# Kernel optimization log

Measured on AMD Instinct MI355X. Metric: run time of the kernel, lower is better.

The kernel has to match this reference:

```python
import jax, jax.numpy as jnp
import numpy as np

D = 1536          # d_model
H = 12            # n_heads // 2 for chunk attention
HD = D // H       # head dim = 128
MAXC = 256        # max_chunks
MAXLEN = 1024     # max_seq_length (size embedding table)
THRESH = 0.5      # boundary threshold (init value of the learned param)


def _gelu(v):
    return jax.nn.gelu(v, approximate=False)  # torch nn.GELU default (erf)


def _cos(a, b):
    # F.cosine_similarity with eps=1e-8
    na = jnp.maximum(jnp.linalg.norm(a, axis=-1), 1e-8)
    nb = jnp.maximum(jnp.linalg.norm(b, axis=-1), 1e-8)
    return jnp.sum(a * b, axis=-1) / (na * nb)


def _interp1d(y, L_out):
    # F.interpolate(mode='linear', align_corners=False) on [B, L_in] -> [B, L_out]
    L_in = y.shape[1]
    src = jnp.clip((jnp.arange(L_out, dtype=y.dtype) + 0.5) * (L_in / L_out) - 0.5, 0.0, L_in - 1)
    i0 = jnp.floor(src).astype(jnp.int32)
    i1 = jnp.minimum(i0 + 1, L_in - 1)
    w = src - i0.astype(y.dtype)
    return y[:, i0] * (1.0 - w) + y[:, i1] * w


def setup_inputs() -> dict:
    key = jax.random.key(0)
    ks = jax.random.split(key, 16)
    B, S = 4, 1024
    rn = lambda k, sh, s=0.02: jax.random.normal(k, sh, dtype=jnp.float32) * s
    return {
        'x': jax.random.normal(ks[0], (B, S, D), dtype=jnp.float32),
        'Wp': rn(ks[1], (D, D)), 'bp': jnp.zeros((D,), jnp.float32),
        'detW1': rn(ks[2], (3, D, 2 * D)), 'detb1': jnp.zeros((3, D), jnp.float32),
        'detW2': rn(ks[3], (3, D // 2, D)), 'detb2': jnp.zeros((3, D // 2), jnp.float32),
        'detW3': rn(ks[4], (3, D // 2)), 'detb3': jnp.zeros((3,), jnp.float32),
        'in_proj_w': rn(ks[5], (3 * D, D)), 'in_proj_b': jnp.zeros((3 * D,), jnp.float32),
        'out_w': rn(ks[6], (D, D)), 'out_b': jnp.zeros((D,), jnp.float32),
        'size_emb': jax.random.normal(ks[7], (MAXLEN, D), dtype=jnp.float32),
        'pos_enc': rn(ks[8], (1, MAXC, D)),
        'procW1': rn(ks[9], (2 * D, D)), 'procb1': jnp.zeros((2 * D,), jnp.float32),
        'procW2': rn(ks[10], (D, 2 * D)), 'procb2': jnp.zeros((D,), jnp.float32),
        'ln_g': jnp.ones((D,), jnp.float32), 'ln_b': jnp.zeros((D,), jnp.float32),
    }


def reference(x, Wp, bp, detW1, detb1, detW2, detb2, detW3, detb3,
              in_proj_w, in_proj_b, out_w, out_b, size_emb, pos_enc,
              procW1, procb1, procW2, procb2, ln_g, ln_b):
    B, S, d = x.shape
    # ---- DynamicSemanticChunker ----
    x_ling = x @ Wp.T + bp
    sims = []
    for scale in (1, 2, 4):
        xs = x_ling[:, ::scale]
        cs = _cos(xs[:, :-1], xs[:, 1:])           # [B, L-1]
        sims.append(_interp1d(cs, S - 1))           # [B, S-1]
    avg_sim = jnp.mean(jnp.stack(sims, 0), axis=0)
    base = 0.5 * (1.0 - avg_sim)
    bi = jnp.concatenate([x[:, :-1], x[:, 1:]], axis=-1)  # [B, S-1, 2d]
    h1 = _gelu(jnp.einsum('bsk,ndk->nbsd', bi, detW1) + detb1[:, None, None, :])
    h2 = _gelu(jnp.einsum('nbsd,nhd->nbsh', h1, detW2) + detb2[:, None, None, :])
    learned = jax.nn.sigmoid(jnp.einsum('nbsh,nh->nbs', h2, detW3) + detb3[:, None, None])
    avg_learned = jnp.mean(learned, axis=0)
    final = 0.6 * base + 0.4 * avg_learned
    boundaries = jnp.concatenate([jnp.ones((B, 1), x.dtype), final], axis=1)  # [B, S]
    # ---- EnhancedChunkLayer.create_chunks ----
    # contiguous ragged chunks == segments between boundary positions
    seg = jnp.cumsum((boundaries > THRESH).astype(jnp.int32), axis=1) - 1      # [B, S]
    # per-chunk MHA == full-seq attention with block-diagonal same-segment mask
    qkv = x @ in_proj_w.T + in_proj_b
    q, k, v = jnp.split(qkv, 3, axis=-1)
    q = q.reshape(B, S, H, HD)
    k = k.reshape(B, S, H, HD)
    v = v.reshape(B, S, H, HD)
    scores = jnp.einsum('bqhd,bkhd->bhqk', q, k) / np.sqrt(HD).astype(np.float32)
    same = (seg[:, None, :, None] == seg[:, None, None, :])                    # [B,1,S,S]
    scores = jnp.where(same, scores, jnp.asarray(-1e9, scores.dtype))
    attn = jax.nn.softmax(scores, axis=-1)
    ctx = jnp.einsum('bhqk,bkhd->bqhd', attn, v).reshape(B, S, d)
    attn_out = ctx @ out_w.T + out_b                                           # [B, S, d]
    # masked segment mean pooling; chunks with id >= MAXC are truncated away
    onehot = (seg[..., None] == jnp.arange(MAXC)).astype(x.dtype)              # [B,S,MAXC]
    sums = jnp.einsum('bsm,bsd->bmd', onehot, attn_out)
    counts = jnp.sum(onehot, axis=1)                                            # [B,MAXC]
    mean = sums / jnp.maximum(counts, 1.0)[..., None]
    clen = jnp.minimum(counts.astype(jnp.int32), MAXLEN - 1)
    sizes = size_emb[clen]                                                      # [B,MAXC,d]
    chunk = jnp.where(counts[..., None] > 0, mean + sizes, 0.0)                 # zero-pad empty
    # ---- pos encoding + chunk_processor (Linear->GELU->Linear->LayerNorm) ----
    chunk = chunk + pos_enc
    h = _gelu(chunk @ procW1.T + procb1)
    y = h @ procW2.T + procb2
    mu = jnp.mean(y, axis=-1, keepdims=True)
    var = jnp.var(y, axis=-1, keepdims=True)
    y = (y - mu) / jnp.sqrt(var + 1e-5) * ln_g + ln_b
    return y  # [B, MAXC, d]
```

## Files before the change

kernel.cpp:

```cpp
#include <hip/hip_runtime.h>
#include <hip/hip_bf16.h>
#include <math.h>

#define D_ 1536
#define S_ 1024
#define B_ 4
#define H_ 12
#define HD_ 128
#define MAXC_ 256

typedef __bf16 bf16x8_t __attribute__((ext_vector_type(8)));
typedef float f32x4_t __attribute__((ext_vector_type(4)));

__device__ __forceinline__ float gelu_f(float v) {
    return 0.5f * v * (1.0f + erff(v / 1.41421356237f));
}

__device__ __forceinline__ void split2(float a, __hip_bfloat16& h, __hip_bfloat16& l) {
    h = __float2bfloat16(a);
    l = __float2bfloat16(a - __bfloat162float(h));
}

__device__ __forceinline__ void xcd_swizzle(int& bx, int& by, int gx, int gy) {
    int nwg = gx * gy;
    int orig = by * gx + bx;
    int xcd = orig & 7;
    int q = nwg >> 3, r = nwg & 7;
    int wg = (xcd < r ? xcd * (q + 1) : r * (q + 1) + (xcd - r) * q) + (orig >> 3);
    bx = wg % gx;
    by = wg / gx;
}

template<int BM, int SPLITA, int SPLITB, int ACT, int OUT, int DBUF>
__global__ __launch_bounds__(256, 2)
void mfma3_gemm(const float* __restrict__ Af, const __hip_bfloat16* __restrict__ Ah,
                const __hip_bfloat16* __restrict__ Al,
                const float* __restrict__ Bf, const __hip_bfloat16* __restrict__ Bh,
                const __hip_bfloat16* __restrict__ Bl,
                const float* __restrict__ bias, int biasStride,
                float* __restrict__ Cf, __hip_bfloat16* __restrict__ Ch, __hip_bfloat16* __restrict__ Cl,
                const float* __restrict__ w3, float* __restrict__ lg,
                int K, int lda, int ldb, int ldc,
                long long aBound, long long azS, long long bzS, long long czS)
{
    constexpr int NB = DBUF ? 2 : 1;
    __shared__ __align__(16) __hip_bfloat16 Ash[NB][BM * 32], Asl[NB][BM * 32];
    __shared__ __align__(16) __hip_bfloat16 Bsh[NB][128 * 32], Bsl[NB][128 * 32];
    const int z = blockIdx.z;
    int bxi = blockIdx.x, byi = blockIdx.y;
    xcd_swizzle(bxi, byi, gridDim.x, gridDim.y);
    const int bm = byi * BM, bn = bxi * 128;
    const int tid = threadIdx.x, lane = tid & 63, wave = tid >> 6;
    const int wm = (BM == 128) ? (wave >> 1) : 0;
    const int wn = (BM == 128) ? (wave & 1) : wave;
    constexpr int NF = (BM == 128) ? 4 : 2;
    constexpr int WC = NF * 16;
    const int fr = lane & 15, kg = lane >> 4;
    f32x4_t acc[4][NF] = {};
    constexpr int RSH = (BM == 128) ? 1 : 2;
    constexpr int NBA = (BM == 128) ? 2 : 1;
    const int ar = tid >> RSH, akb = tid & ((1 << RSH) - 1);
    const int br = tid >> 1, bkb = tid & 1;

    bf16x8_t rAh[NBA], rAl[NBA], rBh[2], rBl[2];
    float4 rAf[NBA][2], rBf[2][2];

    auto load_tile = [&](int k0) {
        #pragma unroll
        for (int j = 0; j < NBA; ++j) {
            int skg = akb * NBA + j;
            long long base = (long long)(bm + ar) * lda + azS * z + k0 + skg * 8;
            if (SPLITA) {
                #pragma unroll
                for (int q = 0; q < 2; ++q) {
                    float4 v = make_float4(0.f, 0.f, 0.f, 0.f);
                    if (base + q * 4 + 4 <= aBound) v = *reinterpret_cast<const float4*>(&Af[base + q * 4]);
                    rAf[j][q] = v;
                }
            } else {
                rAh[j] = *reinterpret_cast<const bf16x8_t*>(&Ah[base]);
                rAl[j] = *reinterpret_cast<const bf16x8_t*>(&Al[base]);
            }
        }
        #pragma unroll
        for (int j = 0; j < 2; ++j) {
            int skg = bkb * 2 + j;
            long long base = (long long)(bn + br) * ldb + bzS * z + k0 + skg * 8;
            if (SPLITB) {
                #pragma unroll
                for (int q = 0; q < 2; ++q)
                    rBf[j][q] = *reinterpret_cast<const float4*>(&Bf[base + q * 4]);
            } else {
                rBh[j] = *reinterpret_cast<const bf16x8_t*>(&Bh[base]);
                rBl[j] = *reinterpret_cast<const bf16x8_t*>(&Bl[base]);
            }
        }
    };

    auto write_tile = [&](int buf) {
        #pragma unroll
        for (int j = 0; j < NBA; ++j) {
            int skg = akb * NBA + j;
            int blk = ar * 4 + (skg ^ ((ar >> 1) & 3));
            if (SPLITA) {
                float av[8];
                *reinterpret_cast<float4*>(&av[0]) = rAf[j][0];
                *reinterpret_cast<float4*>(&av[4]) = rAf[j][1];
                __hip_bfloat16 hh[8], ll[8];
                #pragma unroll
                for (int q = 0; q < 8; ++q) split2(av[q], hh[q], ll[q]);
                *reinterpret_cast<bf16x8_t*>(&Ash[buf][blk * 8]) = *reinterpret_cast<bf16x8_t*>(hh);
                *reinterpret_cast<bf16x8_t*>(&Asl[buf][blk * 8]) = *reinterpret_cast<bf16x8_t*>(ll);
            } else {
                *reinterpret_cast<bf16x8_t*>(&Ash[buf][blk * 8]) = rAh[j];
                *reinterpret_cast<bf16x8_t*>(&Asl[buf][blk * 8]) = rAl[j];
            }
        }
        #pragma unroll
        for (int j = 0; j < 2; ++j) {
            int skg = bkb * 2 + j;
            int blk = br * 4 + (skg ^ ((br >> 1) & 3));
            if (SPLITB) {
                float av[8];
                *reinterpret_cast<float4*>(&av[0]) = rBf[j][0];
                *reinterpret_cast<float4*>(&av[4]) = rBf[j][1];
                __hip_bfloat16 hh[8], ll[8];
                #pragma unroll
                for (int q = 0; q < 8; ++q) split2(av[q], hh[q], ll[q]);
                *reinterpret_cast<bf16x8_t*>(&Bsh[buf][blk * 8]) = *reinterpret_cast<bf16x8_t*>(hh);
                *reinterpret_cast<bf16x8_t*>(&Bsl[buf][blk * 8]) = *reinterpret_cast<bf16x8_t*>(ll);
            } else {
                *reinterpret_cast<bf16x8_t*>(&Bsh[buf][blk * 8]) = rBh[j];
                *reinterpret_cast<bf16x8_t*>(&Bsl[buf][blk * 8]) = rBl[j];
            }
        }
    };

    load_tile(0);
    write_tile(0);
    __syncthreads();
    int cur = 0;

    for (int k0 = 0; k0 < K; k0 += 32) {
        const bool has_next = (k0 + 32) < K;
        if (has_next) load_tile(k0 + 32);

        bf16x8_t fah[4], fal[4], fbh[NF], fbl[NF];
        #pragma unroll
        for (int m = 0; m < 4; ++m) {
            int row = wm * 64 + m * 16 + fr;
            int blk = row * 4 + (kg ^ ((row >> 1) & 3));
            fah[m] = *reinterpret_cast<const bf16x8_t*>(&Ash[cur][blk * 8]);
            fal[m] = *reinterpret_cast<const bf16x8_t*>(&Asl[cur][blk * 8]);
        }
        #pragma unroll
        for (int n = 0; n < NF; ++n) {
            int row = wn * WC + n * 16 + fr;
            int blk = row * 4 + (kg ^ ((row >> 1) & 3));
            fbh[n] = *reinterpret_cast<const bf16x8_t*>(&Bsh[cur][blk * 8]);
            fbl[n] = *reinterpret_cast<const bf16x8_t*>(&Bsl[cur][blk * 8]);
        }
        #pragma unroll
        for (int m = 0; m < 4; ++m)
            #pragma unroll
            for (int n = 0; n < NF; ++n) {
                acc[m][n] = __builtin_amdgcn_mfma_f32_16x16x32_bf16(fah[m], fbh[n], acc[m][n], 0, 0, 0);
                acc[m][n] = __builtin_amdgcn_mfma_f32_16x16x32_bf16(fah[m], fbl[n], acc[m][n], 0, 0, 0);
                acc[m][n] = __builtin_amdgcn_mfma_f32_16x16x32_bf16(fal[m], fbh[n], acc[m][n], 0, 0, 0);
            }

        if (has_next) {
            if (DBUF) {
                write_tile(cur ^ 1);
                __syncthreads();
                cur ^= 1;
            } else {
                __syncthreads();
                write_tile(0);
                __syncthreads();
            }
        }
    }

    const int fq = lane >> 4;
    const float* bp_ = bias + (long long)biasStride * z;

    if constexpr (OUT == 2) {
        float psum[4][4] = {};
        #pragma unroll
        for (int n = 0; n < NF; ++n) {
            int col = bn + wn * WC + n * 16 + fr;
            float bv = bp_[col];
            float wv = w3[(long long)biasStride * z + col];
            #pragma unroll
            for (int m = 0; m < 4; ++m)
                #pragma unroll
                for (int r = 0; r < 4; ++r) {
                    float v = acc[m][n][r] + bv;
                    v = gelu_f(v);
                    psum[m][r] += v * wv;
                }
        }
        #pragma unroll
        for (int m = 0; m < 4; ++m)
            #pragma unroll
            for (int r = 0; r < 4; ++r) {
                float p = psum[m][r];
                p += __shfl_xor(p, 1);
                p += __shfl_xor(p, 2);
                p += __shfl_xor(p, 4);
                p += __shfl_xor(p, 8);
                if (fr == 0) {
                    int row = bm + wm * 64 + m * 16 + fq * 4 + r;
                    atomicAdd(&lg[czS * z + row], p);
                }
            }
        return;
    }

    #pragma unroll
    for (int n = 0; n < NF; ++n) {
        int col = bn + wn * WC + n * 16 + fr;
        float bv = bp_[col];
        #pragma unroll
        for (int m = 0; m < 4; ++m) {
            int row0 = bm + wm * 64 + m * 16 + fq * 4;
            #pragma unroll
            for (int r = 0; r < 4; ++r) {
                float v = acc[m][n][r] + bv;
                if (ACT == 1) v = gelu_f(v);
                long long ci = czS * z + (long long)(row0 + r) * ldc + col;
                if constexpr (OUT == 0) {
                    Cf[ci] = v;
                } else {
                    __hip_bfloat16 hh, ll;
                    split2(v, hh, ll);
                    Ch[ci] = hh; Cl[ci] = ll;
                }
            }
        }
    }
}

template<int ACT, int OUT_BF16>
__global__ __launch_bounds__(256)
void mfma_gemm(const __hip_bfloat16* __restrict__ A, const __hip_bfloat16* __restrict__ Bw,
               const float* __restrict__ bias, void* __restrict__ Cout,
               int M, int N, int K)
{
    __shared__ __align__(16) __hip_bfloat16 As[2][128 * 32];
    __shared__ __align__(16) __hip_bfloat16 Bs[2][128 * 32];
    const int tid = threadIdx.x;
    const int lane = tid & 63;
    const int wave = tid >> 6;
    const int wm = wave >> 1, wn = wave & 1;
    int bxi = blockIdx.x, byi = blockIdx.y;
    xcd_swizzle(bxi, byi, gridDim.x, gridDim.y);
    const int bm = byi * 128, bn = bxi * 128;
    const int srow = tid >> 2;
    const int skg = tid & 3;
    const int fr = lane & 15, kg = lane >> 4;

    f32x4_t acc[4][4] = {};
    bf16x8_t rA[2], rB[2];

    auto load_tile = [&](int k0) {
        #pragma unroll
        for (int it = 0; it < 2; ++it) {
            int r = srow + it * 64;
            rA[it] = *reinterpret_cast<const bf16x8_t*>(&A[(long long)(bm + r) * K + k0 + skg * 8]);
            rB[it] = *reinterpret_cast<const bf16x8_t*>(&Bw[(long long)(bn + r) * K + k0 + skg * 8]);
        }
    };
    auto write_tile = [&](int buf) {
        #pragma unroll
        for (int it = 0; it < 2; ++it) {
            int r = srow + it * 64;
            int blk = r * 4 + (skg ^ ((r >> 1) & 3));
            *reinterpret_cast<bf16x8_t*>(&As[buf][blk * 8]) = rA[it];
            *reinterpret_cast<bf16x8_t*>(&Bs[buf][blk * 8]) = rB[it];
        }
    };

    load_tile(0);
    write_tile(0);
    __syncthreads();
    int cur = 0;

    for (int k0 = 0; k0 < K; k0 += 32) {
        const bool has_next = (k0 + 32) < K;
        if (has_next) load_tile(k0 + 32);

        bf16x8_t af[4], bfr[4];
        #pragma unroll
        for (int m = 0; m < 4; ++m) {
            int row = wm * 64 + m * 16 + fr;
            af[m] = *reinterpret_cast<const bf16x8_t*>(&As[cur][(row * 4 + (kg ^ ((row >> 1) & 3))) * 8]);
        }
        #pragma unroll
        for (int n = 0; n < 4; ++n) {
            int row = wn * 64 + n * 16 + fr;
            bfr[n] = *reinterpret_cast<const bf16x8_t*>(&Bs[cur][(row * 4 + (kg ^ ((row >> 1) & 3))) * 8]);
        }
        #pragma unroll
        for (int m = 0; m < 4; ++m)
            #pragma unroll
            for (int n = 0; n < 4; ++n)
                acc[m][n] = __builtin_amdgcn_mfma_f32_16x16x32_bf16(af[m], bfr[n], acc[m][n], 0, 0, 0);

        if (has_next) {
            write_tile(cur ^ 1);
            __syncthreads();
            cur ^= 1;
        }
    }
    const int fq = lane >> 4;
    #pragma unroll
    for (int n = 0; n < 4; ++n) {
        int col = bn + wn * 64 + n * 16 + fr;
        float bv = bias[col];
        #pragma unroll
        for (int m = 0; m < 4; ++m) {
            int row0 = bm + wm * 64 + m * 16 + fq * 4;
            #pragma unroll
            for (int r = 0; r < 4; ++r) {
                float v = acc[m][n][r] + bv;
                if (ACT == 1) v = gelu_f(v);
                if (OUT_BF16) ((__hip_bfloat16*)Cout)[(long long)(row0 + r) * N + col] = __float2bfloat16(v);
                else          ((float*)Cout)[(long long)(row0 + r) * N + col] = v;
            }
        }
    }
}

__global__ __launch_bounds__(256)
void f2b_kernel(const float* __restrict__ in, __hip_bfloat16* __restrict__ out, int n4)
{
    int i = blockIdx.x * 256 + threadIdx.x;
    if (i >= n4) return;
    float4 v = reinterpret_cast<const float4*>(in)[i];
    __hip_bfloat16 h[4] = { __float2bfloat16(v.x), __float2bfloat16(v.y),
                            __float2bfloat16(v.z), __float2bfloat16(v.w) };
    reinterpret_cast<short4*>(out)[i] = *reinterpret_cast<short4*>(h);
}

__global__ __launch_bounds__(256)
void split_kernel(const float* __restrict__ in, __hip_bfloat16* __restrict__ oh,
                  __hip_bfloat16* __restrict__ ol, int n4)
{
    int i = blockIdx.x * 256 + threadIdx.x;
    if (i >= n4) return;
    float4 v = reinterpret_cast<const float4*>(in)[i];
    __hip_bfloat16 h[4], l[4];
    split2(v.x, h[0], l[0]); split2(v.y, h[1], l[1]);
    split2(v.z, h[2], l[2]); split2(v.w, h[3], l[3]);
    reinterpret_cast<short4*>(oh)[i] = *reinterpret_cast<short4*>(h);
    reinterpret_cast<short4*>(ol)[i] = *reinterpret_cast<short4*>(l);
}

__global__ __launch_bounds__(64)
void cs_kernel(const float* __restrict__ xl, float* __restrict__ cs)
{
    int idx = blockIdx.x;
    int b = blockIdx.y;
    int sc, i, off;
    if (idx < 1023)      { sc = 1; i = idx;        off = 0;    }
    else if (idx < 1534) { sc = 2; i = idx - 1023; off = 1023; }
    else                 { sc = 4; i = idx - 1534; off = 1534; }
    const float* ra = xl + ((long long)b * S_ + (long long)i * sc) * D_;
    const float* rb = ra + (long long)sc * D_;
    int lane = threadIdx.x;
    float dp = 0.f, na = 0.f, nb = 0.f;
    for (int d = lane; d < D_; d += 64) {
        float a = ra[d], c = rb[d];
        dp += a * c; na += a * a; nb += c * c;
    }
    #pragma unroll
    for (int o = 32; o; o >>= 1) {
        dp += __shfl_down(dp, o);
        na += __shfl_down(na, o);
        nb += __shfl_down(nb, o);
    }
    if (lane == 0) {
        float den = fmaxf(sqrtf(na), 1e-8f) * fmaxf(sqrtf(nb), 1e-8f);
        cs[(long long)b * 1789 + off + i] = dp / den;
    }
}

__global__ void final_kernel(const float* __restrict__ cs, const float* __restrict__ logits,
                             const float* __restrict__ b3, float* __restrict__ fin)
{
    int g = blockIdx.x * blockDim.x + threadIdx.x;
    if (g >= B_ * 1023) return;
    int b = g / 1023, t = g % 1023;
    const float* c = cs + (long long)b * 1789;
    float v0 = c[t];
    const float r2 = (float)(511.0 / 1023.0);
    float src2 = fminf(fmaxf(((float)t + 0.5f) * r2 - 0.5f, 0.0f), 510.0f);
    int i0 = (int)floorf(src2);
    int i1 = min(i0 + 1, 510);
    float w2 = src2 - (float)i0;
    float v1 = c[1023 + i0] * (1.0f - w2) + c[1023 + i1] * w2;
    const float r4 = (float)(255.0 / 1023.0);
    float src4 = fminf(fmaxf(((float)t + 0.5f) * r4 - 0.5f, 0.0f), 254.0f);
    int j0 = (int)floorf(src4);
    int j1 = min(j0 + 1, 254);
    float w4 = src4 - (float)j0;
    float v2 = c[1534 + j0] * (1.0f - w4) + c[1534 + j1] * w4;
    float avg = ((v0 + v1) + v2) / 3.0f;
    float base = 0.5f * (1.0f - avg);
    int rr = b * 1024 + t;
    float l0 = 1.0f / (1.0f + expf(-(logits[0 * 4096 + rr] + b3[0])));
    float l1 = 1.0f / (1.0f + expf(-(logits[1 * 4096 + rr] + b3[1])));
    float l2 = 1.0f / (1.0f + expf(-(logits[2 * 4096 + rr] + b3[2])));
    float al = ((l0 + l1) + l2) / 3.0f;
    fin[g] = 0.6f * base + 0.4f * al;
}

__global__ __launch_bounds__(64)
void seg_kernel(const float* __restrict__ fin, int* __restrict__ seg)
{
    int b = blockIdx.x;
    int lane = threadIdx.x;
    int loc[16];
    int cnt = 0;
    #pragma unroll
    for (int i = 0; i < 16; ++i) {
        int t = lane * 16 + i;
        int v = (t >= 1 && fin[b * 1023 + t - 1] > 0.5f) ? 1 : 0;
        cnt += v;
        loc[i] = cnt;
    }
    int inc = cnt;
    #pragma unroll
    for (int o = 1; o < 64; o <<= 1) {
        int u = __shfl_up(inc, o);
        if (lane >= o) inc += u;
    }
    int ex = inc - cnt;
    #pragma unroll
    for (int i = 0; i < 16; ++i) {
        int t = lane * 16 + i;
        seg[b * S_ + t] = ex + loc[i];
    }
}

__global__ void segrange_kernel(const float* __restrict__ fin, const int* __restrict__ seg,
                                int* __restrict__ sstart, int* __restrict__ send,
                                int* __restrict__ cfirst, int* __restrict__ ccount)
{
    int gs = blockIdx.x * blockDim.x + threadIdx.x;
    if (gs >= B_ * S_) return;
    int b = gs / S_, s = gs % S_;
    const float* f = fin + b * 1023;
    int t = s;
    while (t > 0 && !(f[t - 1] > 0.5f)) --t;
    int e = s;
    while (e < 1023 && !(f[e] > 0.5f)) ++e;
    sstart[gs] = t;
    send[gs] = e + 1;
    if (s == t) {
        int m = seg[gs];
        if (m < MAXC_) { cfirst[b * MAXC_ + m] = t; ccount[b * MAXC_ + m] = e + 1 - t; }
    }
}

__global__ __launch_bounds__(256)
void attn_kernel(const __hip_bfloat16* __restrict__ qkv, const int* __restrict__ sstart,
                 const int* __restrict__ send, __hip_bfloat16* __restrict__ ctx)
{
    int gs = blockIdx.x;
    int h = blockIdx.y * 4 + threadIdx.y;
    int lane = threadIdx.x;
    int b = gs >> 10;
    const __hip_bfloat16* qrow = qkv + (long long)gs * 4608 + h * HD_;
    float q0 = __bfloat162float(qrow[lane]), q1 = __bfloat162float(qrow[lane + 64]);
    int st = sstart[gs], en = send[gs];
    float m = -INFINITY, l = 0.f, a0 = 0.f, a1 = 0.f;
    for (int t = st; t < en; ++t) {
        long long krow = ((long long)(b * S_ + t)) * 4608 + 1536 + h * HD_;
        float p = q0 * __bfloat162float(qkv[krow + lane]) + q1 * __bfloat162float(qkv[krow + lane + 64]);
        #pragma unroll
        for (int o = 32; o; o >>= 1) p += __shfl_xor(p, o);
        p = p / 11.3137084989847603904f;
        float nm = fmaxf(m, p);
        float scale = expf(m - nm);
        float w = expf(p - nm);
        long long vrow = ((long long)(b * S_ + t)) * 4608 + 3072 + h * HD_;
        l = l * scale + w;
        a0 = a0 * scale + w * __bfloat162float(qkv[vrow + lane]);
        a1 = a1 * scale + w * __bfloat162float(qkv[vrow + lane + 64]);
        m = nm;
    }
    float inv = 1.0f / l;
    ctx[(long long)gs * D_ + h * HD_ + lane] = __float2bfloat16(a0 * inv);
    ctx[(long long)gs * D_ + h * HD_ + lane + 64] = __float2bfloat16(a1 * inv);
}

__global__ __launch_bounds__(256)
void chunk_kernel(const float* __restrict__ attn_out, const int* __restrict__ cfirst,
                  const int* __restrict__ ccount, const float* __restrict__ size_emb,
                  const float* __restrict__ pos_enc, __hip_bfloat16* __restrict__ chunk)
{
    int m = blockIdx.x, b = blockIdx.y;
    int cnt = ccount[b * MAXC_ + m];
    for (int d = threadIdx.x; d < D_; d += 256) {
        float v;
        if (cnt > 0) {
            int first = cfirst[b * MAXC_ + m];
            float ssum = 0.f;
            for (int t = 0; t < cnt; ++t)
                ssum += attn_out[((long long)(b * S_ + first + t)) * D_ + d];
            float mean = ssum / (float)cnt;
            int clen = min(cnt, 1023);
            v = mean + size_emb[(long long)clen * D_ + d];
        } else {
            v = 0.f;
        }
        v += pos_enc[m * D_ + d];
        chunk[((long long)(b * MAXC_ + m)) * D_ + d] = __float2bfloat16(v);
    }
}

__global__ __launch_bounds__(256)
void ln_kernel(const float* __restrict__ y0, const float* __restrict__ g,
               const float* __restrict__ bb, float* __restrict__ out)
{
    int r = blockIdx.x;
    const float* row = y0 + (long long)r * D_;
    float loc[6];
    float s = 0.f;
    #pragma unroll
    for (int i = 0; i < 6; ++i) { loc[i] = row[threadIdx.x + i * 256]; s += loc[i]; }
    __shared__ float red[256];
    red[threadIdx.x] = s; __syncthreads();
    for (int o = 128; o; o >>= 1) { if (threadIdx.x < o) red[threadIdx.x] += red[threadIdx.x + o]; __syncthreads(); }
    float mu = red[0] / 1536.0f;
    __syncthreads();
    float s2 = 0.f;
    #pragma unroll
    for (int i = 0; i < 6; ++i) { float d = loc[i] - mu; s2 += d * d; }
    red[threadIdx.x] = s2; __syncthreads();
    for (int o = 128; o; o >>= 1) { if (threadIdx.x < o) red[threadIdx.x] += red[threadIdx.x + o]; __syncthreads(); }
    float var = red[0] / 1536.0f;
    float inv = 1.0f / sqrtf(var + 1e-5f);
    #pragma unroll
    for (int i = 0; i < 6; ++i) {
        int d = threadIdx.x + i * 256;
        out[(long long)r * D_ + d] = (loc[i] - mu) * inv * g[d] + bb[d];
    }
}

extern "C" void kernel_launch(void* const* d_in, const int* in_sizes, int n_in,
                              void* d_out, int out_size, void* d_ws, size_t ws_size,
                              hipStream_t stream)
{
    const float* x         = (const float*)d_in[0];
    const float* Wp        = (const float*)d_in[1];
    const float* bp        = (const float*)d_in[2];
    const float* detW1     = (const float*)d_in[3];
    const float* detb1     = (const float*)d_in[4];
    const float* detW2     = (const float*)d_in[5];
    const float* detb2     = (const float*)d_in[6];
    const float* detW3     = (const float*)d_in[7];
    const float* detb3     = (const float*)d_in[8];
    const float* in_proj_w = (const float*)d_in[9];
    const float* in_proj_b = (const float*)d_in[10];
    const float* out_w     = (const float*)d_in[11];
    const float* out_b     = (const float*)d_in[12];
    const float* size_emb  = (const float*)d_in[13];
    const float* pos_enc   = (const float*)d_in[14];
    const float* procW1    = (const float*)d_in[15];
    const float* procb1    = (const float*)d_in[16];
    const float* procW2    = (const float*)d_in[17];
    const float* procb2    = (const float*)d_in[18];
    const float* ln_g      = (const float*)d_in[19];
    const float* ln_b      = (const float*)d_in[20];
    float* out = (float*)d_out;

    const bool big = ws_size >= (size_t)192 * 1024 * 1024;

    char* ws = (char*)d_ws;
    float*          xlingf = (float*)(ws + 0);
    __hip_bfloat16* Wph    = (__hip_bfloat16*)(ws + 25165824);
    __hip_bfloat16* Wpl    = (__hip_bfloat16*)(ws + 29884416);
    __hip_bfloat16* h1h    = (__hip_bfloat16*)(ws + 0);
    __hip_bfloat16* h1l    = (__hip_bfloat16*)(ws + 37748736);
    __hip_bfloat16* W1h_s  = (__hip_bfloat16*)(ws + 75497472);
    __hip_bfloat16* W1l_s  = (__hip_bfloat16*)(ws + 94371840);
    __hip_bfloat16* W2h_s  = (__hip_bfloat16*)(ws + 75497472);
    __hip_bfloat16* W2l_s  = (__hip_bfloat16*)(ws + 82575360);
    __hip_bfloat16* xh     = (__hip_bfloat16*)(ws + 75497472);
    __hip_bfloat16* xl     = (__hip_bfloat16*)(ws + 88082432);
    __hip_bfloat16* W1h_b  = (__hip_bfloat16*)(ws + 125829120);
    __hip_bfloat16* W1l_b  = (__hip_bfloat16*)(ws + 154140672);
    __hip_bfloat16* W2h_b  = (__hip_bfloat16*)(ws + 125829120);
    __hip_bfloat16* W2l_b  = (__hip_bfloat16*)(ws + 132907008);
    __hip_bfloat16* xb_s       = (__hip_bfloat16*)(ws + 0);
    __hip_bfloat16* in_proj_wb = (__hip_bfloat16*)(ws + 12582912);
    __hip_bfloat16* qkvb       = (__hip_bfloat16*)(ws + 26738688);
    __hip_bfloat16* ctxb       = (__hip_bfloat16*)(ws + 64487424);
    __hip_bfloat16* out_wb     = (__hip_bfloat16*)(ws + 12582912);
    float*          attno      = (float*)(ws + 77070336);
    __hip_bfloat16* chunkb     = (__hip_bfloat16*)(ws + 0);
    __hip_bfloat16* procW1b    = (__hip_bfloat16*)(ws + 3145728);
    __hip_bfloat16* hmidb      = (__hip_bfloat16*)(ws + 12582912);
    __hip_bfloat16* procW2b    = (__hip_bfloat16*)(ws + 18874368);
    float*          y0         = (float*)(ws + 28311552);
    char* sm = ws + 113246208;
    float* csb    = (float*)(sm + 0);
    float* logits = (float*)(sm + 28672);
    float* fin    = (float*)(sm + 77824);
    int*   seg    = (int*)  (sm + 94208);
    int*   sstart = (int*)  (sm + 110592);
    int*   send   = (int*)  (sm + 126976);
    int*   cfirst = (int*)  (sm + 143360);
    int*   ccount = (int*)  (sm + 147456);

    const long long SLICE_W1 = 4718592LL;
    const long long SLICE_W2 = 1179648LL;
    const long long H1_Z     = 6291456LL;

    split_kernel<<<(2359296 / 4 + 255) / 256, 256, 0, stream>>>(Wp, Wph, Wpl, 2359296 / 4);
    if (big)
        split_kernel<<<(6291456 / 4 + 255) / 256, 256, 0, stream>>>(x, xh, xl, 6291456 / 4);

    if (big)
        mfma3_gemm<128, 0, 0, 0, 0, 1><<<dim3(12, 32, 1), 256, 0, stream>>>(
            nullptr, xh, xl, nullptr, Wph, Wpl, bp, 0,
            xlingf, nullptr, nullptr, nullptr, nullptr,
            1536, 1536, 1536, 1536, 0LL, 0LL, 0LL, 0LL);
    else
        mfma3_gemm<64, 1, 0, 0, 0, 1><<<dim3(12, 64, 1), 256, 0, stream>>>(
            x, nullptr, nullptr, nullptr, Wph, Wpl, bp, 0,
            xlingf, nullptr, nullptr, nullptr, nullptr,
            1536, 1536, 1536, 1536, 6291456LL, 0LL, 0LL, 0LL);
    cs_kernel<<<dim3(1789, 4), 64, 0, stream>>>(xlingf, csb);

    if (big) {
        split_kernel<<<(14155776 / 4 + 255) / 256, 256, 0, stream>>>(detW1, W1h_b, W1l_b, 14155776 / 4);
        mfma3_gemm<128, 0, 0, 1, 1, 0><<<dim3(12, 32, 3), 256, 0, stream>>>(
            nullptr, xh, xl, nullptr, W1h_b, W1l_b, detb1, 1536,
            nullptr, h1h, h1l, nullptr, nullptr,
            3072, 1536, 3072, 1536, 0LL, 0LL, SLICE_W1, H1_Z);
    } else {
        split_kernel<<<(2 * 4718592 / 4 + 255) / 256, 256, 0, stream>>>(detW1, W1h_s, W1l_s, 2 * 4718592 / 4);
        mfma3_gemm<128, 1, 0, 1, 1, 0><<<dim3(12, 32, 2), 256, 0, stream>>>(
            x, nullptr, nullptr, nullptr, W1h_s, W1l_s, detb1, 1536,
            nullptr, h1h, h1l, nullptr, nullptr,
            3072, 1536, 3072, 1536, 6291456LL, 0LL, SLICE_W1, H1_Z);
        split_kernel<<<(4718592 / 4 + 255) / 256, 256, 0, stream>>>(detW1 + 2 * SLICE_W1, W1h_s, W1l_s, 4718592 / 4);
        mfma3_gemm<64, 1, 0, 1, 1, 0><<<dim3(12, 64, 1), 256, 0, stream>>>(
            x, nullptr, nullptr, nullptr, W1h_s, W1l_s, detb1 + 2 * 1536, 1536,
            nullptr, h1h + 2 * H1_Z, h1l + 2 * H1_Z, nullptr, nullptr,
            3072, 1536, 3072, 1536, 6291456LL, 0LL, 0LL, 0LL);
    }

    __hip_bfloat16* W2h = big ? W2h_b : W2h_s;
    __hip_bfloat16* W2l = big ? W2l_b : W2l_s;
    split_kernel<<<(3538944 / 4 + 255) / 256, 256, 0, stream>>>(detW2, W2h, W2l, 3538944 / 4);
    hipMemsetAsync(logits, 0, 3 * 4096 * sizeof(float), stream);
    mfma3_gemm<128, 0, 0, 1, 2, 1><<<dim3(6, 32, 3), 256, 0, stream>>>(
        nullptr, h1h, h1l, nullptr, W2h, W2l, detb2, 768,
        nullptr, nullptr, nullptr, detW3, logits,
        1536, 1536, 1536, 768, 0LL, H1_Z, SLICE_W2, 4096LL);

    final_kernel<<<16, 256, 0, stream>>>(csb, logits, detb3, fin);
    seg_kernel<<<4, 64, 0, stream>>>(fin, seg);
    hipMemsetAsync(ccount, 0, B_ * MAXC_ * sizeof(int), stream);
    segrange_kernel<<<16, 256, 0, stream>>>(fin, seg, sstart, send, cfirst, ccount);

    const __hip_bfloat16* xbf;
    if (big) {
        xbf = xh;
    } else {
        f2b_kernel<<<(4096 * 1536 / 4 + 255) / 256, 256, 0, stream>>>(x, xb_s, 4096 * 1536 / 4);
        xbf = xb_s;
    }
    f2b_kernel<<<(4608 * 1536 / 4 + 255) / 256, 256, 0, stream>>>(in_proj_w, in_proj_wb, 4608 * 1536 / 4);
    mfma_gemm<0, 1><<<dim3(36, 32), 256, 0, stream>>>(xbf, in_proj_wb, in_proj_b, qkvb, 4096, 4608, 1536);

    attn_kernel<<<dim3(4096, 3), dim3(64, 4), 0, stream>>>(qkvb, sstart, send, ctxb);

    f2b_kernel<<<(1536 * 1536 / 4 + 255) / 256, 256, 0, stream>>>(out_w, out_wb, 1536 * 1536 / 4);
    mfma_gemm<0, 0><<<dim3(12, 32), 256, 0, stream>>>(ctxb, out_wb, out_b, attno, 4096, 1536, 1536);

    chunk_kernel<<<dim3(256, 4), 256, 0, stream>>>(attno, cfirst, ccount, size_emb, pos_enc, chunkb);

    f2b_kernel<<<(3072 * 1536 / 4 + 255) / 256, 256, 0, stream>>>(procW1, procW1b, 3072 * 1536 / 4);
    mfma_gemm<1, 1><<<dim3(24, 8), 256, 0, stream>>>(chunkb, procW1b, procb1, hmidb, 1024, 3072, 1536);
    f2b_kernel<<<(1536 * 3072 / 4 + 255) / 256, 256, 0, stream>>>(procW2, procW2b, 1536 * 3072 / 4);
    mfma_gemm<0, 0><<<dim3(12, 8), 256, 0, stream>>>(hmidb, procW2b, procb2, y0, 1024, 1536, 3072);

    ln_kernel<<<1024, 256, 0, stream>>>(y0, ln_g, ln_b, out);
}
```

Baseline: 1.098 ms.

## Prefetch two K-tiles ahead into registers for single-buffered GEMM path

For the non-double-buffered GEMM variant, global loads now go into two alternating register sets, so each tile is fetched two iterations before it is written to shared memory. This hides more global-load latency behind the MFMA work without needing a second LDS buffer. The double-buffered path keeps the same schedule, rewritten with macros. The cost is more registers per thread, which could lower occupancy or cause spills.

After: 1.159 ms. 5.5% more time.

```diff
diff --git a/kernel.cpp b/kernel.cpp
--- a/kernel.cpp
+++ b/kernel.cpp
@@ -62,103 +62,99 @@
     const int ar = tid >> RSH, akb = tid & ((1 << RSH) - 1);
     const int br = tid >> 1, bkb = tid & 1;
 
-    bf16x8_t rAh[NBA], rAl[NBA], rBh[2], rBl[2];
-    float4 rAf[NBA][2], rBf[2][2];
-
-    auto load_tile = [&](int k0) {
-        #pragma unroll
-        for (int j = 0; j < NBA; ++j) {
-            int skg = akb * NBA + j;
-            long long base = (long long)(bm + ar) * lda + azS * z + k0 + skg * 8;
-            if (SPLITA) {
-                #pragma unroll
-                for (int q = 0; q < 2; ++q) {
-                    float4 v = make_float4(0.f, 0.f, 0.f, 0.f);
-                    if (base + q * 4 + 4 <= aBound) v = *reinterpret_cast<const float4*>(&Af[base + q * 4]);
-                    rAf[j][q] = v;
-                }
-            } else {
-                rAh[j] = *reinterpret_cast<const bf16x8_t*>(&Ah[base]);
-                rAl[j] = *reinterpret_cast<const bf16x8_t*>(&Al[base]);
-            }
-        }
-        #pragma unroll
-        for (int j = 0; j < 2; ++j) {
-            int skg = bkb * 2 + j;
-            long long base = (long long)(bn + br) * ldb + bzS * z + k0 + skg * 8;
-            if (SPLITB) {
-                #pragma unroll
-                for (int q = 0; q < 2; ++q)
-                    rBf[j][q] = *reinterpret_cast<const float4*>(&Bf[base + q * 4]);
-            } else {
-                rBh[j] = *reinterpret_cast<const bf16x8_t*>(&Bh[base]);
-                rBl[j] = *reinterpret_cast<const bf16x8_t*>(&Bl[base]);
-            }
-        }
-    };
-
-    auto write_tile = [&](int buf) {
-        #pragma unroll
-        for (int j = 0; j < NBA; ++j) {
-            int skg = akb * NBA + j;
-            int blk = ar * 4 + (skg ^ ((ar >> 1) & 3));
-            if (SPLITA) {
-                float av[8];
-                *reinterpret_cast<float4*>(&av[0]) = rAf[j][0];
-                *reinterpret_cast<float4*>(&av[4]) = rAf[j][1];
-                __hip_bfloat16 hh[8], ll[8];
-                #pragma unroll
-                for (int q = 0; q < 8; ++q) split2(av[q], hh[q], ll[q]);
-                *reinterpret_cast<bf16x8_t*>(&Ash[buf][blk * 8]) = *reinterpret_cast<bf16x8_t*>(hh);
-                *reinterpret_cast<bf16x8_t*>(&Asl[buf][blk * 8]) = *reinterpret_cast<bf16x8_t*>(ll);
-            } else {
-                *reinterpret_cast<bf16x8_t*>(&Ash[buf][blk * 8]) = rAh[j];
-                *reinterpret_cast<bf16x8_t*>(&Asl[buf][blk * 8]) = rAl[j];
-            }
-        }
-        #pragma unroll
-        for (int j = 0; j < 2; ++j) {
-            int skg = bkb * 2 + j;
-            int blk = br * 4 + (skg ^ ((br >> 1) & 3));
-            if (SPLITB) {
-                float av[8];
-                *reinterpret_cast<float4*>(&av[0]) = rBf[j][0];
-                *reinterpret_cast<float4*>(&av[4]) = rBf[j][1];
-                __hip_bfloat16 hh[8], ll[8];
-                #pragma unroll
-                for (int q = 0; q < 8; ++q) split2(av[q], hh[q], ll[q]);
-                *reinterpret_cast<bf16x8_t*>(&Bsh[buf][blk * 8]) = *reinterpret_cast<bf16x8_t*>(hh);
-                *reinterpret_cast<bf16x8_t*>(&Bsl[buf][blk * 8]) = *reinterpret_cast<bf16x8_t*>(ll);
-            } else {
-                *reinterpret_cast<bf16x8_t*>(&Bsh[buf][blk * 8]) = rBh[j];
-                *reinterpret_cast<bf16x8_t*>(&Bsl[buf][blk * 8]) = rBl[j];
-            }
-        }
-    };
-
-    load_tile(0);
-    write_tile(0);
-    __syncthreads();
-    int cur = 0;
-
-    for (int k0 = 0; k0 < K; k0 += 32) {
-        const bool has_next = (k0 + 32) < K;
-        if (has_next) load_tile(k0 + 32);
-
+    bf16x8_t rAh0[NBA], rAl0[NBA], rBh0[2], rBl0[2];
+    bf16x8_t rAh1[NBA], rAl1[NBA], rBh1[2], rBl1[2];
+    float4 rAf0[NBA][2], rBf0[2][2];
+    float4 rAf1[NBA][2], rBf1[2][2];
+
+#define LOAD_TILE(k0, rAh_, rAl_, rAf_, rBh_, rBl_, rBf_)                                       \
+    {                                                                                           \
+        _Pragma("unroll")                                                                       \
+        for (int j = 0; j < NBA; ++j) {                                                         \
+            int skg = akb * NBA + j;                                                            \
+            long long base = (long long)(bm + ar) * lda + azS * z + (k0) + skg * 8;             \
+            if (SPLITA) {                                                                       \
+                _Pragma("unroll")                                                               \
+                for (int q = 0; q < 2; ++q) {                                                   \
+                    float4 v = make_float4(0.f, 0.f, 0.f, 0.f);                                 \
+                    if (base + q * 4 + 4 <= aBound) v = *reinterpret_cast<const float4*>(&Af[base + q * 4]); \
+                    rAf_[j][q] = v;                                                             \
+                }                                                                               \
+            } else {                                                                            \
+                rAh_[j] = *reinterpret_cast<const bf16x8_t*>(&Ah[base]);                        \
+                rAl_[j] = *reinterpret_cast<const bf16x8_t*>(&Al[base]);                        \
+            }                                                                                   \
+        }                                                                                       \
+        _Pragma("unroll")                                                                       \
+        for (int j = 0; j < 2; ++j) {                                                           \
+            int skg = bkb * 2 + j;                                                              \
+            long long base = (long long)(bn + br) * ldb + bzS * z + (k0) + skg * 8;             \
+            if (SPLITB) {                                                                       \
+                _Pragma("unroll")                                                               \
+                for (int q = 0; q < 2; ++q)                                                     \
+                    rBf_[j][q] = *reinterpret_cast<const float4*>(&Bf[base + q * 4]);           \
+            } else {                                                                            \
+                rBh_[j] = *reinterpret_cast<const bf16x8_t*>(&Bh[base]);                        \
+                rBl_[j] = *reinterpret_cast<const bf16x8_t*>(&Bl[base]);                        \
+            }                                                                                   \
+        }                                                                                       \
+    }
+
+#define WRITE_TILE(buf, rAh_, rAl_, rAf_, rBh_, rBl_, rBf_)                                     \
+    {                                                                                           \
+        _Pragma("unroll")                                                                       \
+        for (int j = 0; j < NBA; ++j) {                                                         \
+            int skg = akb * NBA + j;                                                            \
+            int blk = ar * 4 + (skg ^ ((ar >> 1) & 3));                                         \
+            if (SPLITA) {                                                                       \
+                float av[8];                                                                    \
+                *reinterpret_cast<float4*>(&av[0]) = rAf_[j][0];                                \
+                *reinterpret_cast<float4*>(&av[4]) = rAf_[j][1];                                \
+                __hip_bfloat16 hh[8], ll[8];                                                    \
+                _Pragma("unroll")                                                               \
+                for (int q = 0; q < 8; ++q) split2(av[q], hh[q], ll[q]);                        \
+                *reinterpret_cast<bf16x8_t*>(&Ash[buf][blk * 8]) = *reinterpret_cast<bf16x8_t*>(hh); \
+                *reinterpret_cast<bf16x8_t*>(&Asl[buf][blk * 8]) = *reinterpret_cast<bf16x8_t*>(ll); \
+            } else {                                                                            \
+                *reinterpret_cast<bf16x8_t*>(&Ash[buf][blk * 8]) = rAh_[j];                     \
+                *reinterpret_cast<bf16x8_t*>(&Asl[buf][blk * 8]) = rAl_[j];                     \
+            }                                                                                   \
+        }                                                                                       \
+        _Pragma("unroll")                                                                       \
+        for (int j = 0; j < 2; ++j) {                                                           \
+            int skg = bkb * 2 + j;                                                              \
+            int blk = br * 4 + (skg ^ ((br >> 1) & 3));                                         \
+            if (SPLITB) {                                                                       \
+                float av[8];                                                                    \
+                *reinterpret_cast<float4*>(&av[0]) = rBf_[j][0];                                \
+                *reinterpret_cast<float4*>(&av[4]) = rBf_[j][1];                                \
+                __hip_bfloat16 hh[8], ll[8];                                                    \
+                _Pragma("unroll")                                                               \
+                for (int q = 0; q < 8; ++q) split2(av[q], hh[q], ll[q]);                        \
+                *reinterpret_cast<bf16x8_t*>(&Bsh[buf][blk * 8]) = *reinterpret_cast<bf16x8_t*>(hh); \
+                *reinterpret_cast<bf16x8_t*>(&Bsl[buf][blk * 8]) = *reinterpret_cast<bf16x8_t*>(ll); \
+            } else {                                                                            \
+                *reinterpret_cast<bf16x8_t*>(&Bsh[buf][blk * 8]) = rBh_[j];                     \
+                *reinterpret_cast<bf16x8_t*>(&Bsl[buf][blk * 8]) = rBl_[j];                     \
+            }                                                                                   \
+        }                                                                                       \
+    }
+
+    auto compute = [&](int buf) {
         bf16x8_t fah[4], fal[4], fbh[NF], fbl[NF];
         #pragma unroll
         for (int m = 0; m < 4; ++m) {
             int row = wm * 64 + m * 16 + fr;
             int blk = row * 4 + (kg ^ ((row >> 1) & 3));
-            fah[m] = *reinterpret_cast<const bf16x8_t*>(&Ash[cur][blk * 8]);
-            fal[m] = *reinterpret_cast<const bf16x8_t*>(&Asl[cur][blk * 8]);
+            fah[m] = *reinterpret_cast<const bf16x8_t*>(&Ash[buf][blk * 8]);
+            fal[m] = *reinterpret_cast<const bf16x8_t*>(&Asl[buf][blk * 8]);
         }
         #pragma unroll
         for (int n = 0; n < NF; ++n) {
             int row = wn * WC + n * 16 + fr;
             int blk = row * 4 + (kg ^ ((row >> 1) & 3));
-            fbh[n] = *reinterpret_cast<const bf16x8_t*>(&Bsh[cur][blk * 8]);
-            fbl[n] = *reinterpret_cast<const bf16x8_t*>(&Bsl[cur][blk * 8]);
+            fbh[n] = *reinterpret_cast<const bf16x8_t*>(&Bsh[buf][blk * 8]);
+            fbl[n] = *reinterpret_cast<const bf16x8_t*>(&Bsl[buf][blk * 8]);
         }
         #pragma unroll
         for (int m = 0; m < 4; ++m)
@@ -168,19 +164,49 @@
                 acc[m][n] = __builtin_amdgcn_mfma_f32_16x16x32_bf16(fah[m], fbl[n], acc[m][n], 0, 0, 0);
                 acc[m][n] = __builtin_amdgcn_mfma_f32_16x16x32_bf16(fal[m], fbh[n], acc[m][n], 0, 0, 0);
             }
-
-        if (has_next) {
-            if (DBUF) {
-                write_tile(cur ^ 1);
+    };
+
+    if constexpr (DBUF) {
+        LOAD_TILE(0, rAh0, rAl0, rAf0, rBh0, rBl0, rBf0);
+        WRITE_TILE(0, rAh0, rAl0, rAf0, rBh0, rBl0, rBf0);
+        __syncthreads();
+        int cur = 0;
+        for (int k0 = 0; k0 < K; k0 += 32) {
+            const bool has_next = (k0 + 32) < K;
+            if (has_next) LOAD_TILE(k0 + 32, rAh0, rAl0, rAf0, rBh0, rBl0, rBf0);
+            compute(cur);
+            if (has_next) {
+                if (cur) { WRITE_TILE(0, rAh0, rAl0, rAf0, rBh0, rBl0, rBf0); }
+                else     { WRITE_TILE(1, rAh0, rAl0, rAf0, rBh0, rBl0, rBf0); }
                 __syncthreads();
                 cur ^= 1;
-            } else {
-                __syncthreads();
-                write_tile(0);
-                __syncthreads();
             }
         }
-    }
+    } else {
+        const int nk = K >> 5;
+        LOAD_TILE(0, rAh0, rAl0, rAf0, rBh0, rBl0, rBf0);
+        WRITE_TILE(0, rAh0, rAl0, rAf0, rBh0, rBl0, rBf0);
+        if (nk > 1) LOAD_TILE(32, rAh1, rAl1, rAf1, rBh1, rBl1, rBf1);
+        __syncthreads();
+        int i = 0;
+        while (true) {
+            if (i + 2 < nk) LOAD_TILE((i + 2) << 5, rAh0, rAl0, rAf0, rBh0, rBl0, rBf0);
+            compute(0);
+            if (i + 1 >= nk) break;
+            __syncthreads();
+            WRITE_TILE(0, rAh1, rAl1, rAf1, rBh1, rBl1, rBf1);
+            __syncthreads();
+            if (i + 3 < nk) LOAD_TILE((i + 3) << 5, rAh1, rAl1, rAf1, rBh1, rBl1, rBf1);
+            compute(0);
+            if (i + 2 >= nk) break;
+            __syncthreads();
+            WRITE_TILE(0, rAh0, rAl0, rAf0, rBh0, rBl0, rBf0);
+            __syncthreads();
+            i += 2;
+        }
+    }
+#undef LOAD_TILE
+#undef WRITE_TILE
 
     const int fq = lane >> 4;
     const float* bp_ = bias + (long long)biasStride * z;
```

## Stage GEMM tiles via direct global-to-LDS loads, single-buffered

Applied to the files above, without the earlier changes.

Replaces the register-staged double-buffered tile loads in the MFMA GEMM with global_load_lds instructions that write global data straight into shared memory. The XOR swizzle is applied to the source address instead of the destination. This removes VGPR staging and LDS store instructions and halves shared memory use. In exchange it drops the double buffering, so each k-step waits on its own load with two barriers and loses load/compute overlap.

Result: faster. 1.069 ms, median of 4 (-2.7%).

```diff
diff --git a/kernel.cpp b/kernel.cpp
--- a/kernel.cpp
+++ b/kernel.cpp
@@ -248,8 +248,8 @@
                const float* __restrict__ bias, void* __restrict__ Cout,
                int M, int N, int K)
 {
-    __shared__ __align__(16) __hip_bfloat16 As[2][128 * 32];
-    __shared__ __align__(16) __hip_bfloat16 Bs[2][128 * 32];
+    __shared__ __align__(16) __hip_bfloat16 As[128 * 32];
+    __shared__ __align__(16) __hip_bfloat16 Bs[128 * 32];
     const int tid = threadIdx.x;
     const int lane = tid & 63;
     const int wave = tid >> 6;
@@ -257,50 +257,43 @@
     int bxi = blockIdx.x, byi = blockIdx.y;
     xcd_swizzle(bxi, byi, gridDim.x, gridDim.y);
     const int bm = byi * 128, bn = bxi * 128;
-    const int srow = tid >> 2;
-    const int skg = tid & 3;
     const int fr = lane & 15, kg = lane >> 4;
 
     f32x4_t acc[4][4] = {};
-    bf16x8_t rA[2], rB[2];
-
-    auto load_tile = [&](int k0) {
-        #pragma unroll
-        for (int it = 0; it < 2; ++it) {
-            int r = srow + it * 64;
-            rA[it] = *reinterpret_cast<const bf16x8_t*>(&A[(long long)(bm + r) * K + k0 + skg * 8]);
-            rB[it] = *reinterpret_cast<const bf16x8_t*>(&Bw[(long long)(bn + r) * K + k0 + skg * 8]);
+
+    auto stage = [&](int k0) {
+        #pragma unroll
+        for (int c = 0; c < 2; ++c) {
+            int idx = (wave * 2 + c) * 64 + lane;
+            int row = idx >> 2, slot = idx & 3;
+            int srck = slot ^ ((row >> 1) & 3);
+            const __hip_bfloat16* ga = &A[(long long)(bm + row) * K + k0 + srck * 8];
+            const __hip_bfloat16* gb = &Bw[(long long)(bn + row) * K + k0 + srck * 8];
+            __builtin_amdgcn_global_load_lds(
+                (const __attribute__((address_space(1))) unsigned int*)ga,
+                (__attribute__((address_space(3))) unsigned int*)&As[(wave * 2 + c) * 512],
+                16, 0, 0);
+            __builtin_amdgcn_global_load_lds(
+                (const __attribute__((address_space(1))) unsigned int*)gb,
+                (__attribute__((address_space(3))) unsigned int*)&Bs[(wave * 2 + c) * 512],
+                16, 0, 0);
         }
     };
-    auto write_tile = [&](int buf) {
-        #pragma unroll
-        for (int it = 0; it < 2; ++it) {
-            int r = srow + it * 64;
-            int blk = r * 4 + (skg ^ ((r >> 1) & 3));
-            *reinterpret_cast<bf16x8_t*>(&As[buf][blk * 8]) = rA[it];
-            *reinterpret_cast<bf16x8_t*>(&Bs[buf][blk * 8]) = rB[it];
-        }
-    };
-
-    load_tile(0);
-    write_tile(0);
-    __syncthreads();
-    int cur = 0;
 
     for (int k0 = 0; k0 < K; k0 += 32) {
-        const bool has_next = (k0 + 32) < K;
-        if (has_next) load_tile(k0 + 32);
+        stage(k0);
+        __syncthreads();
 
         bf16x8_t af[4], bfr[4];
         #pragma unroll
         for (int m = 0; m < 4; ++m) {
             int row = wm * 64 + m * 16 + fr;
-            af[m] = *reinterpret_cast<const bf16x8_t*>(&As[cur][(row * 4 + (kg ^ ((row >> 1) & 3))) * 8]);
+            af[m] = *reinterpret_cast<const bf16x8_t*>(&As[(row * 4 + (kg ^ ((row >> 1) & 3))) * 8]);
         }
         #pragma unroll
         for (int n = 0; n < 4; ++n) {
             int row = wn * 64 + n * 16 + fr;
-            bfr[n] = *reinterpret_cast<const bf16x8_t*>(&Bs[cur][(row * 4 + (kg ^ ((row >> 1) & 3))) * 8]);
+            bfr[n] = *reinterpret_cast<const bf16x8_t*>(&Bs[(row * 4 + (kg ^ ((row >> 1) & 3))) * 8]);
         }
         #pragma unroll
         for (int m = 0; m < 4; ++m)
@@ -308,11 +301,7 @@
             for (int n = 0; n < 4; ++n)
                 acc[m][n] = __builtin_amdgcn_mfma_f32_16x16x32_bf16(af[m], bfr[n], acc[m][n], 0, 0, 0);
 
-        if (has_next) {
-            write_tile(cur ^ 1);
-            __syncthreads();
-            cur ^= 1;
-        }
+        __syncthreads();
     }
     const int fq = lane >> 4;
     #pragma unroll
```
